# Optimization experiments

Measured on AMD Instinct MI355X. Metric: run time of the kernel, lower is better.

Reference implementation:

```python
import jax, jax.numpy as jnp
import numpy as np

NEG_MASK = -9e15
ALPHA = 0.2  # LeakyReLU negative slope


def _gat_layer(h, adj, W, a):
    # h: [B,K,Fin], adj: [B,K,K], W: [Fin,F], a: [2F]
    Wh = jnp.einsum('bki,io->bko', h, W)            # [B,K,F]
    F = Wh.shape[-1]
    a_src, a_dst = a[:F], a[F:]
    # e_ij = LeakyReLU(a . [Wh_i || Wh_j]) = LeakyReLU(Wh_i.a_src + Wh_j.a_dst)
    f_src = Wh @ a_src                              # [B,K]
    f_dst = Wh @ a_dst                              # [B,K]
    e = jax.nn.leaky_relu(f_src[:, :, None] + f_dst[:, None, :], ALPHA)  # [B,K,K]
    e = jnp.where(adj > 0, e, NEG_MASK)
    att = jax.nn.softmax(e, axis=2)                 # softmax over neighbors j
    # dropout is identity in eval mode (training=False)
    h_prime = jnp.einsum('bkj,bjo->bko', att, Wh)   # [B,K,F]
    return jax.nn.elu(h_prime)


def setup_inputs() -> dict:
    key = jax.random.key(0)
    ks = jax.random.split(key, 6)
    B, K, Fin, H, Fout = 128, 512, 224, 64, 32
    x = jax.random.normal(ks[0], (B, K, Fin), dtype=jnp.float32)
    adj = jax.random.randint(ks[1], (B, K, K), 0, 2, dtype=jnp.int32)
    W1 = jax.random.normal(ks[2], (Fin, H), dtype=jnp.float32) * (1.0 / np.sqrt(Fin))
    a1 = jax.random.normal(ks[3], (2 * H,), dtype=jnp.float32) * 0.1
    W2 = jax.random.normal(ks[4], (H, Fout), dtype=jnp.float32) * (1.0 / np.sqrt(H))
    a2 = jax.random.normal(ks[5], (2 * Fout,), dtype=jnp.float32) * 0.1
    return {"x": x, "adj": adj, "W1": W1, "a1": a1, "W2": W2, "a2": a2}


def reference(x, adj, W1, a1, W2, a2):
    h = _gat_layer(x, adj, W1, a1)   # conv1: in -> hidden
    h = _gat_layer(h, adj, W2, a2)   # conv2: hidden -> out
    return h
```

## Files before the change

kernel.cpp:

```cpp
#include <hip/hip_runtime.h>
#include <stdint.h>


#define B_   128
#define K_   512
#define FIN  224
#define H1   64
#define H2   32

typedef float    f32x4 __attribute__((ext_vector_type(4)));
typedef short    s16x8 __attribute__((ext_vector_type(8)));
typedef unsigned short u16;

__device__ __forceinline__ u16 f2bf(float f){
  uint32_t u = __float_as_uint(f);
  u += 0x7FFFu + ((u >> 16) & 1u);
  return (u16)(u >> 16);
}
__device__ __forceinline__ float bf2f(u16 h){ return __uint_as_float(((uint32_t)h) << 16); }

__device__ __forceinline__ int fragoff(int o, int k, int NO){
  return (((k >> 5) * (NO >> 4) + (o >> 4)) << 9) + (((o & 15) + (((k & 31) >> 3) << 4)) << 3) + (k & 7);
}

__global__ __launch_bounds__(256) void k_bitmask(const int* __restrict__ adj, uint32_t* __restrict__ bits2){
  const int t = threadIdx.x;
#pragma unroll 4
  for (int it = 0; it < 16; ++it){
    const size_t q = (size_t)blockIdx.x * 4096 + it * 256 + t;
    int4 v = reinterpret_cast<const int4*>(adj)[q];
    uint32_t nib = (v.x != 0 ? 1u : 0u) | (v.y != 0 ? 2u : 0u) | (v.z != 0 ? 4u : 0u) | (v.w != 0 ? 8u : 0u);
    uint32_t val = nib << ((t & 7) * 4);
    val |= __shfl_xor(val, 1);
    val |= __shfl_xor(val, 2);
    val |= __shfl_xor(val, 4);
    if ((t & 7) == 0){
      const size_t qw = q >> 3;
      const int st = (int)(qw & 15), i = (int)((qw >> 4) & 511), b = (int)(qw >> 13);
      bits2[((size_t)(b * 16 + st) << 9) + i] = val;
    }
  }
}

__global__ __launch_bounds__(256) void k_prep(const float* __restrict__ W1, const float* __restrict__ W2,
                                              u16* __restrict__ W1F, u16* __restrict__ W2F){
  int t = blockIdx.x * 256 + threadIdx.x;
  if (t < FIN * H1){ int k = t / H1, o = t % H1; W1F[fragoff(o, k, H1)] = f2bf(W1[t]); }
  else { int u = t - FIN * H1; if (u < H1 * H2){ int k = u / H2, o = u % H2; W2F[fragoff(o, k, H2)] = f2bf(W2[u]); } }
}

template<int KD, int NO, bool AF32>
__global__ __launch_bounds__(256) void k_gemm(const void* __restrict__ Ain, const u16* __restrict__ WF,
                                              const float* __restrict__ avec,
                                              u16* __restrict__ WhF, float* __restrict__ fs, float* __restrict__ fd){
  const int tid = threadIdx.x;
  const int wid = tid >> 6, lane = tid & 63;
  const int g = lane >> 4, lr = lane & 15;
  const size_t row0 = (size_t)blockIdx.x * 64;
  const size_t arow = row0 + 16 * wid + lr;

  f32x4 acc[NO / 16];
#pragma unroll
  for (int c = 0; c < NO/16; ++c) acc[c] = (f32x4){0.f, 0.f, 0.f, 0.f};

#pragma unroll
  for (int s = 0; s < KD / 32; ++s){
    const int k0 = s * 32 + 8 * g;
    s16x8 af;
    if (AF32){
      const float* A = (const float*)Ain;
      float4 v0 = *(const float4*)(A + arow * KD + k0);
      float4 v1 = *(const float4*)(A + arow * KD + k0 + 4);
      af[0] = (short)f2bf(v0.x); af[1] = (short)f2bf(v0.y); af[2] = (short)f2bf(v0.z); af[3] = (short)f2bf(v0.w);
      af[4] = (short)f2bf(v1.x); af[5] = (short)f2bf(v1.y); af[6] = (short)f2bf(v1.z); af[7] = (short)f2bf(v1.w);
    } else {
      af = *(const s16x8*)((const u16*)Ain + arow * KD + k0);
    }
#pragma unroll
    for (int c = 0; c < NO/16; ++c){
      const s16x8 bf = *(const s16x8*)(WF + ((s * (NO/16) + c) << 9) + lane * 8);
      acc[c] = __builtin_amdgcn_mfma_f32_16x16x32_bf16(af, bf, acc[c], 0, 0, 0);
    }
  }

  const size_t b = row0 >> 9;
  const int krow0 = (int)(row0 & 511) + 16 * wid + 4 * g;
  float fsp[4] = {0.f,0.f,0.f,0.f}, fdp[4] = {0.f,0.f,0.f,0.f};
#pragma unroll
  for (int c = 0; c < NO/16; ++c){
    const int o = 16 * c + lr;
    const float as = avec[o], ad = avec[NO + o];
#pragma unroll
    for (int r = 0; r < 4; ++r){ fsp[r] += acc[c][r] * as; fdp[r] += acc[c][r] * ad; }
    uint2 pk;
    pk.x = (uint32_t)f2bf(acc[c][0]) | ((uint32_t)f2bf(acc[c][1]) << 16);
    pk.y = (uint32_t)f2bf(acc[c][2]) | ((uint32_t)f2bf(acc[c][3]) << 16);
    *(uint2*)(WhF + b * (NO * 512) + fragoff(o, krow0, NO)) = pk;
  }
#pragma unroll
  for (int m = 1; m < 16; m <<= 1){
#pragma unroll
    for (int r = 0; r < 4; ++r){ fsp[r] += __shfl_xor(fsp[r], m); fdp[r] += __shfl_xor(fdp[r], m); }
  }
  if (lr == 0){
#pragma unroll
    for (int r = 0; r < 4; ++r){
      size_t row = row0 + 16 * wid + 4 * g + r;
      fs[row] = fsp[r]; fd[row] = fdp[r];
    }
  }
}

template<int NO, bool OUTBF>
__global__ __launch_bounds__(256) void k_attn(const u16* __restrict__ WhF, const float* __restrict__ fsv,
                                              const float* __restrict__ fdv, const uint32_t* __restrict__ bits2,
                                              void* __restrict__ outp){
  const int tid = threadIdx.x;
  const int wid = tid >> 6, lane = tid & 63;
  const int g = lane >> 4, lr = lane & 15;
  const int b = blockIdx.x >> 3;
  const int i0 = (blockIdx.x & 7) * 64;
  const int irow = i0 + 16 * wid + lr;
  const float fsr = fsv[(size_t)b * K_ + irow];
  const float* fdb = fdv + (size_t)b * K_;
  const uint32_t* bb = bits2 + ((size_t)b * 16 << 9);
  const u16* whb = WhF + (size_t)b * (NO * 512);

  f32x4 acc[NO / 16];
#pragma unroll
  for (int c = 0; c < NO/16; ++c) acc[c] = (f32x4){0.f, 0.f, 0.f, 0.f};
  float lsum = 0.f;

  for (int st = 0; st < 16; ++st){
    const int j0 = st * 32 + 8 * g;
    const uint32_t byte = (bb[(st << 9) + irow] >> (8 * g)) & 0xFFu;
    float4 fd0 = *(const float4*)(fdb + j0);
    float4 fd1 = *(const float4*)(fdb + j0 + 4);
    float pv[8] = { fd0.x, fd0.y, fd0.z, fd0.w, fd1.x, fd1.y, fd1.z, fd1.w };
    s16x8 bp;
    float lacc = 0.f;
#pragma unroll
    for (int e = 0; e < 8; ++e){
      float sc = fsr + pv[e];
      sc = fmaxf(sc, 0.2f * sc);
      float pe = __expf(sc - 8.0f);
      pe = ((byte >> e) & 1u) ? pe : 0.f;
      u16 h = f2bf(pe);
      bp[e] = (short)h;
      lacc += bf2f(h);
    }
    lsum += lacc;
#pragma unroll
    for (int c = 0; c < NO/16; ++c){
      const s16x8 aw = *(const s16x8*)(whb + ((st * (NO/16) + c) << 9) + lane * 8);
      acc[c] = __builtin_amdgcn_mfma_f32_16x16x32_bf16(aw, bp, acc[c], 0, 0, 0);
    }
  }

  lsum += __shfl_xor(lsum, 16);
  lsum += __shfl_xor(lsum, 32);
  const float inv = 1.0f / lsum;

#pragma unroll
  for (int c = 0; c < NO/16; ++c){
    float v[4];
#pragma unroll
    for (int r = 0; r < 4; ++r){
      float t = acc[c][r] * inv;
      v[r] = t > 0.f ? t : (__expf(t) - 1.0f);
    }
    const size_t base = ((size_t)b * K_ + irow) * NO + 16 * c + 4 * g;
    if (OUTBF){
      uint2 pk;
      pk.x = (uint32_t)f2bf(v[0]) | ((uint32_t)f2bf(v[1]) << 16);
      pk.y = (uint32_t)f2bf(v[2]) | ((uint32_t)f2bf(v[3]) << 16);
      *(uint2*)((u16*)outp + base) = pk;
    } else {
      *(float4*)((float*)outp + base) = (float4){v[0], v[1], v[2], v[3]};
    }
  }
}

extern "C" void kernel_launch(void* const* d_in, const int* in_sizes, int n_in,
                              void* d_out, int out_size, void* d_ws, size_t ws_size,
                              hipStream_t stream){
  const float* x   = (const float*)d_in[0];
  const int*   adj = (const int*)  d_in[1];
  const float* W1  = (const float*)d_in[2];
  const float* a1  = (const float*)d_in[3];
  const float* W2  = (const float*)d_in[4];
  const float* a2  = (const float*)d_in[5];
  float* out = (float*)d_out;

  char* ws = (char*)d_ws;
  u16*      WhF1 = (u16*)     (ws);
  u16*      h1   = (u16*)     (ws + 8388608);
  u16*      WhF2 = (u16*)     (ws + 16777216);
  uint32_t* bits = (uint32_t*)(ws + 20971520);
  float*    fs1  = (float*)   (ws + 25165824);
  float*    fd1  = (float*)   (ws + 25427968);
  float*    fs2  = (float*)   (ws + 25690112);
  float*    fd2  = (float*)   (ws + 25952256);
  u16*      W1F  = (u16*)     (ws + 26214400);
  u16*      W2F  = (u16*)     (ws + 26243072);

  k_bitmask<<<dim3(2048), dim3(256), 0, stream>>>(adj, bits);
  k_prep   <<<dim3(64),   dim3(256), 0, stream>>>(W1, W2, W1F, W2F);
  k_gemm<FIN, H1, true >  <<<dim3(1024), dim3(256), 0, stream>>>((const void*)x,  W1F, a1, WhF1, fs1, fd1);
  k_attn<H1, true >       <<<dim3(1024), dim3(256), 0, stream>>>(WhF1, fs1, fd1, bits, (void*)h1);
  k_gemm<H1,  H2, false>  <<<dim3(1024), dim3(256), 0, stream>>>((const void*)h1, W2F, a2, WhF2, fs2, fd2);
  k_attn<H2, false>       <<<dim3(1024), dim3(256), 0, stream>>>(WhF2, fs2, fd2, bits, (void*)out);
}
```

Measured before the change: 293.9 us.

## Fuse both GAT layers into one per-batch kernel keeping intermediates in LDS

```diff
diff --git a/kernel.cpp b/kernel.cpp
--- a/kernel.cpp
+++ b/kernel.cpp
@@ -2,7 +2,6 @@
 #include <stdint.h>
 
 
-#define B_   128
 #define K_   512
 #define FIN  224
 #define H1   64
@@ -23,160 +22,300 @@
   return (((k >> 5) * (NO >> 4) + (o >> 4)) << 9) + (((o & 15) + (((k & 31) >> 3) << 4)) << 3) + (k & 7);
 }
 
-__global__ __launch_bounds__(256) void k_bitmask(const int* __restrict__ adj, uint32_t* __restrict__ bits2){
-  const int t = threadIdx.x;
+
+__global__ __launch_bounds__(1024, 4) void k_gat(const float* __restrict__ x, const int* __restrict__ adj,
+                                                 const float* __restrict__ W1, const float* __restrict__ a1,
+                                                 const float* __restrict__ W2, const float* __restrict__ a2,
+                                                 float* __restrict__ out){
+  __shared__ __align__(16) char arena[147456];
+  u16*      WhS      = (u16*)     (arena);
+  uint32_t* bits_tmp = (uint32_t*)(arena + 65536);
+  u16*      W1F      = (u16*)     (arena + 98304);
+  u16*      h1S      = (u16*)     (arena + 65536);
+  u16*      W2F      = (u16*)     (arena + 139264);
+  float*    fs_s     = (float*)   (arena + 143360);
+  float*    fd_s     = (float*)   (arena + 145408);
+
+  const int tid = threadIdx.x;
+  const int w = tid >> 6, lane = tid & 63;
+  const int g = lane >> 4, lr = lane & 15;
+  const int b = blockIdx.x;
+
+  for (int e = tid; e < FIN * H1; e += 1024){
+    const int k = e >> 6, o = e & 63;
+    W1F[fragoff(o, k, H1)] = f2bf(W1[e]);
+  }
+#pragma unroll
+  for (int p = 0; p < 2; ++p){
+    const int e = tid + p * 1024;
+    const int k = e >> 5, o = e & 31;
+    W2F[fragoff(o, k, H2)] = f2bf(W2[e]);
+  }
+  {
+    const int4* ap = reinterpret_cast<const int4*>(adj) + (size_t)b * 65536;
 #pragma unroll 4
-  for (int it = 0; it < 16; ++it){
-    const size_t q = (size_t)blockIdx.x * 4096 + it * 256 + t;
-    int4 v = reinterpret_cast<const int4*>(adj)[q];
-    uint32_t nib = (v.x != 0 ? 1u : 0u) | (v.y != 0 ? 2u : 0u) | (v.z != 0 ? 4u : 0u) | (v.w != 0 ? 8u : 0u);
-    uint32_t val = nib << ((t & 7) * 4);
-    val |= __shfl_xor(val, 1);
-    val |= __shfl_xor(val, 2);
-    val |= __shfl_xor(val, 4);
-    if ((t & 7) == 0){
-      const size_t qw = q >> 3;
-      const int st = (int)(qw & 15), i = (int)((qw >> 4) & 511), b = (int)(qw >> 13);
-      bits2[((size_t)(b * 16 + st) << 9) + i] = val;
-    }
-  }
-}
-
-__global__ __launch_bounds__(256) void k_prep(const float* __restrict__ W1, const float* __restrict__ W2,
-                                              u16* __restrict__ W1F, u16* __restrict__ W2F){
-  int t = blockIdx.x * 256 + threadIdx.x;
-  if (t < FIN * H1){ int k = t / H1, o = t % H1; W1F[fragoff(o, k, H1)] = f2bf(W1[t]); }
-  else { int u = t - FIN * H1; if (u < H1 * H2){ int k = u / H2, o = u % H2; W2F[fragoff(o, k, H2)] = f2bf(W2[u]); } }
-}
-
-template<int KD, int NO, bool AF32>
-__global__ __launch_bounds__(256) void k_gemm(const void* __restrict__ Ain, const u16* __restrict__ WF,
-                                              const float* __restrict__ avec,
-                                              u16* __restrict__ WhF, float* __restrict__ fs, float* __restrict__ fd){
-  const int tid = threadIdx.x;
-  const int wid = tid >> 6, lane = tid & 63;
-  const int g = lane >> 4, lr = lane & 15;
-  const size_t row0 = (size_t)blockIdx.x * 64;
-  const size_t arow = row0 + 16 * wid + lr;
-
-  f32x4 acc[NO / 16];
-#pragma unroll
-  for (int c = 0; c < NO/16; ++c) acc[c] = (f32x4){0.f, 0.f, 0.f, 0.f};
-
-#pragma unroll
-  for (int s = 0; s < KD / 32; ++s){
-    const int k0 = s * 32 + 8 * g;
-    s16x8 af;
-    if (AF32){
-      const float* A = (const float*)Ain;
-      float4 v0 = *(const float4*)(A + arow * KD + k0);
-      float4 v1 = *(const float4*)(A + arow * KD + k0 + 4);
-      af[0] = (short)f2bf(v0.x); af[1] = (short)f2bf(v0.y); af[2] = (short)f2bf(v0.z); af[3] = (short)f2bf(v0.w);
-      af[4] = (short)f2bf(v1.x); af[5] = (short)f2bf(v1.y); af[6] = (short)f2bf(v1.z); af[7] = (short)f2bf(v1.w);
-    } else {
-      af = *(const s16x8*)((const u16*)Ain + arow * KD + k0);
-    }
-#pragma unroll
-    for (int c = 0; c < NO/16; ++c){
-      const s16x8 bf = *(const s16x8*)(WF + ((s * (NO/16) + c) << 9) + lane * 8);
-      acc[c] = __builtin_amdgcn_mfma_f32_16x16x32_bf16(af, bf, acc[c], 0, 0, 0);
-    }
-  }
-
-  const size_t b = row0 >> 9;
-  const int krow0 = (int)(row0 & 511) + 16 * wid + 4 * g;
-  float fsp[4] = {0.f,0.f,0.f,0.f}, fdp[4] = {0.f,0.f,0.f,0.f};
-#pragma unroll
-  for (int c = 0; c < NO/16; ++c){
-    const int o = 16 * c + lr;
-    const float as = avec[o], ad = avec[NO + o];
-#pragma unroll
-    for (int r = 0; r < 4; ++r){ fsp[r] += acc[c][r] * as; fdp[r] += acc[c][r] * ad; }
-    uint2 pk;
-    pk.x = (uint32_t)f2bf(acc[c][0]) | ((uint32_t)f2bf(acc[c][1]) << 16);
-    pk.y = (uint32_t)f2bf(acc[c][2]) | ((uint32_t)f2bf(acc[c][3]) << 16);
-    *(uint2*)(WhF + b * (NO * 512) + fragoff(o, krow0, NO)) = pk;
-  }
-#pragma unroll
-  for (int m = 1; m < 16; m <<= 1){
-#pragma unroll
-    for (int r = 0; r < 4; ++r){ fsp[r] += __shfl_xor(fsp[r], m); fdp[r] += __shfl_xor(fdp[r], m); }
-  }
-  if (lr == 0){
-#pragma unroll
-    for (int r = 0; r < 4; ++r){
-      size_t row = row0 + 16 * wid + 4 * g + r;
-      fs[row] = fsp[r]; fd[row] = fdp[r];
-    }
-  }
-}
-
-template<int NO, bool OUTBF>
-__global__ __launch_bounds__(256) void k_attn(const u16* __restrict__ WhF, const float* __restrict__ fsv,
-                                              const float* __restrict__ fdv, const uint32_t* __restrict__ bits2,
-                                              void* __restrict__ outp){
-  const int tid = threadIdx.x;
-  const int wid = tid >> 6, lane = tid & 63;
-  const int g = lane >> 4, lr = lane & 15;
-  const int b = blockIdx.x >> 3;
-  const int i0 = (blockIdx.x & 7) * 64;
-  const int irow = i0 + 16 * wid + lr;
-  const float fsr = fsv[(size_t)b * K_ + irow];
-  const float* fdb = fdv + (size_t)b * K_;
-  const uint32_t* bb = bits2 + ((size_t)b * 16 << 9);
-  const u16* whb = WhF + (size_t)b * (NO * 512);
-
-  f32x4 acc[NO / 16];
-#pragma unroll
-  for (int c = 0; c < NO/16; ++c) acc[c] = (f32x4){0.f, 0.f, 0.f, 0.f};
-  float lsum = 0.f;
-
-  for (int st = 0; st < 16; ++st){
-    const int j0 = st * 32 + 8 * g;
-    const uint32_t byte = (bb[(st << 9) + irow] >> (8 * g)) & 0xFFu;
-    float4 fd0 = *(const float4*)(fdb + j0);
-    float4 fd1 = *(const float4*)(fdb + j0 + 4);
-    float pv[8] = { fd0.x, fd0.y, fd0.z, fd0.w, fd1.x, fd1.y, fd1.z, fd1.w };
-    s16x8 bp;
-    float lacc = 0.f;
-#pragma unroll
-    for (int e = 0; e < 8; ++e){
-      float sc = fsr + pv[e];
-      sc = fmaxf(sc, 0.2f * sc);
-      float pe = __expf(sc - 8.0f);
-      pe = ((byte >> e) & 1u) ? pe : 0.f;
-      u16 h = f2bf(pe);
-      bp[e] = (short)h;
-      lacc += bf2f(h);
-    }
-    lsum += lacc;
-#pragma unroll
-    for (int c = 0; c < NO/16; ++c){
-      const s16x8 aw = *(const s16x8*)(whb + ((st * (NO/16) + c) << 9) + lane * 8);
-      acc[c] = __builtin_amdgcn_mfma_f32_16x16x32_bf16(aw, bp, acc[c], 0, 0, 0);
-    }
-  }
-
-  lsum += __shfl_xor(lsum, 16);
-  lsum += __shfl_xor(lsum, 32);
-  const float inv = 1.0f / lsum;
-
-#pragma unroll
-  for (int c = 0; c < NO/16; ++c){
-    float v[4];
-#pragma unroll
-    for (int r = 0; r < 4; ++r){
-      float t = acc[c][r] * inv;
-      v[r] = t > 0.f ? t : (__expf(t) - 1.0f);
-    }
-    const size_t base = ((size_t)b * K_ + irow) * NO + 16 * c + 4 * g;
-    if (OUTBF){
-      uint2 pk;
-      pk.x = (uint32_t)f2bf(v[0]) | ((uint32_t)f2bf(v[1]) << 16);
-      pk.y = (uint32_t)f2bf(v[2]) | ((uint32_t)f2bf(v[3]) << 16);
-      *(uint2*)((u16*)outp + base) = pk;
-    } else {
-      *(float4*)((float*)outp + base) = (float4){v[0], v[1], v[2], v[3]};
+    for (int it = 0; it < 64; ++it){
+      const int q = it * 1024 + tid;
+      int4 v = ap[q];
+      uint32_t nib = (v.x != 0 ? 1u : 0u) | (v.y != 0 ? 2u : 0u) | (v.z != 0 ? 4u : 0u) | (v.w != 0 ? 8u : 0u);
+      uint32_t val = nib << ((q & 7) * 4);
+      val |= __shfl_xor(val, 1);
+      val |= __shfl_xor(val, 2);
+      val |= __shfl_xor(val, 4);
+      if ((tid & 7) == 0)
+        bits_tmp[((q & 127) >> 3) * K_ + (q >> 7)] = val;
+    }
+  }
+  __syncthreads();
+
+  {
+    f32x4 acc[2][4];
+#pragma unroll
+    for (int h = 0; h < 2; ++h)
+#pragma unroll
+      for (int c = 0; c < 4; ++c) acc[h][c] = (f32x4){0.f,0.f,0.f,0.f};
+
+    for (int s = 0; s < FIN / 32; ++s){
+      s16x8 af[2];
+#pragma unroll
+      for (int h = 0; h < 2; ++h){
+        const float* xr = x + ((size_t)b * K_ + 32 * w + 16 * h + lr) * FIN + s * 32 + 8 * g;
+        float4 v0 = *(const float4*)xr;
+        float4 v1 = *(const float4*)(xr + 4);
+        af[h][0]=(short)f2bf(v0.x); af[h][1]=(short)f2bf(v0.y); af[h][2]=(short)f2bf(v0.z); af[h][3]=(short)f2bf(v0.w);
+        af[h][4]=(short)f2bf(v1.x); af[h][5]=(short)f2bf(v1.y); af[h][6]=(short)f2bf(v1.z); af[h][7]=(short)f2bf(v1.w);
+      }
+#pragma unroll
+      for (int c = 0; c < 4; ++c){
+        const s16x8 bf = *(const s16x8*)&W1F[((s * 4 + c) << 9) + lane * 8];
+#pragma unroll
+        for (int h = 0; h < 2; ++h)
+          acc[h][c] = __builtin_amdgcn_mfma_f32_16x16x32_bf16(af[h], bf, acc[h][c], 0, 0, 0);
+      }
+    }
+    float fsp[2][4] = {{0}}, fdp[2][4] = {{0}};
+#pragma unroll
+    for (int h = 0; h < 2; ++h)
+#pragma unroll
+      for (int c = 0; c < 4; ++c){
+        const int o = 16 * c + lr;
+        const float as = a1[o], ad = a1[H1 + o];
+#pragma unroll
+        for (int r = 0; r < 4; ++r){ fsp[h][r] += acc[h][c][r] * as; fdp[h][r] += acc[h][c][r] * ad; }
+        uint2 pk;
+        pk.x = (uint32_t)f2bf(acc[h][c][0]) | ((uint32_t)f2bf(acc[h][c][1]) << 16);
+        pk.y = (uint32_t)f2bf(acc[h][c][2]) | ((uint32_t)f2bf(acc[h][c][3]) << 16);
+        const int off = ((w * 4 + c) << 9) + ((lr + 16 * (2 * h + (g >> 1))) << 3) + 4 * (g & 1);
+        *(uint2*)&WhS[off] = pk;
+      }
+#pragma unroll
+    for (int m = 1; m < 16; m <<= 1)
+#pragma unroll
+      for (int h = 0; h < 2; ++h)
+#pragma unroll
+        for (int r = 0; r < 4; ++r){ fsp[h][r] += __shfl_xor(fsp[h][r], m); fdp[h][r] += __shfl_xor(fdp[h][r], m); }
+    if (lr == 0){
+#pragma unroll
+      for (int h = 0; h < 2; ++h)
+#pragma unroll
+        for (int r = 0; r < 4; ++r){
+          const int row = 32 * w + 16 * h + 4 * g + r;
+          fs_s[row] = fsp[h][r]; fd_s[row] = fdp[h][r];
+        }
+    }
+  }
+
+  uint32_t bw[2][4] = {{0,0,0,0},{0,0,0,0}};
+#pragma unroll
+  for (int h = 0; h < 2; ++h){
+    const int row = 32 * w + 16 * h + lr;
+#pragma unroll
+    for (int st = 0; st < 16; ++st){
+      const uint32_t byte = (bits_tmp[st * K_ + row] >> (8 * g)) & 0xFFu;
+      bw[h][st >> 2] |= byte << (8 * (st & 3));
+    }
+  }
+  __syncthreads();
+
+  {
+    f32x4 acc[2][4];
+#pragma unroll
+    for (int h = 0; h < 2; ++h)
+#pragma unroll
+      for (int c = 0; c < 4; ++c) acc[h][c] = (f32x4){0.f,0.f,0.f,0.f};
+    float lsum[2] = {0.f, 0.f};
+    const float fsr[2] = { fs_s[32 * w + lr], fs_s[32 * w + 16 + lr] };
+
+    for (int st = 0; st < 16; ++st){
+      const int j0 = 32 * st + 8 * g;
+      float4 fd0 = *(const float4*)&fd_s[j0];
+      float4 fd1 = *(const float4*)&fd_s[j0 + 4];
+      const float pv[8] = { fd0.x, fd0.y, fd0.z, fd0.w, fd1.x, fd1.y, fd1.z, fd1.w };
+      s16x8 bp[2];
+#pragma unroll
+      for (int h = 0; h < 2; ++h){
+        const uint32_t byte = (bw[h][st >> 2] >> (8 * (st & 3))) & 0xFFu;
+        float lacc = 0.f;
+#pragma unroll
+        for (int e = 0; e < 8; ++e){
+          float sc = fsr[h] + pv[e];
+          sc = fmaxf(sc, 0.2f * sc);
+          float pe = __expf(sc - 8.0f);
+          pe = ((byte >> e) & 1u) ? pe : 0.f;
+          u16 hh = f2bf(pe);
+          bp[h][e] = (short)hh;
+          lacc += bf2f(hh);
+        }
+        lsum[h] += lacc;
+      }
+#pragma unroll
+      for (int c = 0; c < 4; ++c){
+        const s16x8 aw = *(const s16x8*)&WhS[((st * 4 + c) << 9) + lane * 8];
+#pragma unroll
+        for (int h = 0; h < 2; ++h)
+          acc[h][c] = __builtin_amdgcn_mfma_f32_16x16x32_bf16(aw, bp[h], acc[h][c], 0, 0, 0);
+      }
+    }
+    float inv[2];
+#pragma unroll
+    for (int h = 0; h < 2; ++h){
+      lsum[h] += __shfl_xor(lsum[h], 16);
+      lsum[h] += __shfl_xor(lsum[h], 32);
+      inv[h] = 1.0f / lsum[h];
+    }
+#pragma unroll
+    for (int h = 0; h < 2; ++h){
+      const int irow = 32 * w + 16 * h + lr;
+#pragma unroll
+      for (int c = 0; c < 4; ++c){
+        float v[4];
+#pragma unroll
+        for (int r = 0; r < 4; ++r){
+          float t = acc[h][c][r] * inv[h];
+          v[r] = t > 0.f ? t : (__expf(t) - 1.0f);
+        }
+        uint2 pk;
+        pk.x = (uint32_t)f2bf(v[0]) | ((uint32_t)f2bf(v[1]) << 16);
+        pk.y = (uint32_t)f2bf(v[2]) | ((uint32_t)f2bf(v[3]) << 16);
+        *(uint2*)&h1S[irow * 72 + 16 * c + 4 * g] = pk;
+      }
+    }
+  }
+  __syncthreads();
+
+  {
+    f32x4 acc[2][2];
+#pragma unroll
+    for (int h = 0; h < 2; ++h)
+#pragma unroll
+      for (int c = 0; c < 2; ++c) acc[h][c] = (f32x4){0.f,0.f,0.f,0.f};
+
+#pragma unroll
+    for (int s = 0; s < H1 / 32; ++s){
+      s16x8 af[2];
+#pragma unroll
+      for (int h = 0; h < 2; ++h)
+        af[h] = *(const s16x8*)&h1S[(32 * w + 16 * h + lr) * 72 + s * 32 + 8 * g];
+#pragma unroll
+      for (int c = 0; c < 2; ++c){
+        const s16x8 bf = *(const s16x8*)&W2F[((s * 2 + c) << 9) + lane * 8];
+#pragma unroll
+        for (int h = 0; h < 2; ++h)
+          acc[h][c] = __builtin_amdgcn_mfma_f32_16x16x32_bf16(af[h], bf, acc[h][c], 0, 0, 0);
+      }
+    }
+    float fsp[2][4] = {{0}}, fdp[2][4] = {{0}};
+#pragma unroll
+    for (int h = 0; h < 2; ++h)
+#pragma unroll
+      for (int c = 0; c < 2; ++c){
+        const int o = 16 * c + lr;
+        const float as = a2[o], ad = a2[H2 + o];
+#pragma unroll
+        for (int r = 0; r < 4; ++r){ fsp[h][r] += acc[h][c][r] * as; fdp[h][r] += acc[h][c][r] * ad; }
+        uint2 pk;
+        pk.x = (uint32_t)f2bf(acc[h][c][0]) | ((uint32_t)f2bf(acc[h][c][1]) << 16);
+        pk.y = (uint32_t)f2bf(acc[h][c][2]) | ((uint32_t)f2bf(acc[h][c][3]) << 16);
+        const int off = ((w * 2 + c) << 9) + ((lr + 16 * (2 * h + (g >> 1))) << 3) + 4 * (g & 1);
+        *(uint2*)&WhS[off] = pk;
+      }
+#pragma unroll
+    for (int m = 1; m < 16; m <<= 1)
+#pragma unroll
+      for (int h = 0; h < 2; ++h)
+#pragma unroll
+        for (int r = 0; r < 4; ++r){ fsp[h][r] += __shfl_xor(fsp[h][r], m); fdp[h][r] += __shfl_xor(fdp[h][r], m); }
+    if (lr == 0){
+#pragma unroll
+      for (int h = 0; h < 2; ++h)
+#pragma unroll
+        for (int r = 0; r < 4; ++r){
+          const int row = 32 * w + 16 * h + 4 * g + r;
+          fs_s[row] = fsp[h][r]; fd_s[row] = fdp[h][r];
+        }
+    }
+  }
+  __syncthreads();
+
+  {
+    f32x4 acc[2][2];
+#pragma unroll
+    for (int h = 0; h < 2; ++h)
+#pragma unroll
+      for (int c = 0; c < 2; ++c) acc[h][c] = (f32x4){0.f,0.f,0.f,0.f};
+    float lsum[2] = {0.f, 0.f};
+    const float fsr[2] = { fs_s[32 * w + lr], fs_s[32 * w + 16 + lr] };
+
+    for (int st = 0; st < 16; ++st){
+      const int j0 = 32 * st + 8 * g;
+      float4 fd0 = *(const float4*)&fd_s[j0];
+      float4 fd1 = *(const float4*)&fd_s[j0 + 4];
+      const float pv[8] = { fd0.x, fd0.y, fd0.z, fd0.w, fd1.x, fd1.y, fd1.z, fd1.w };
+      s16x8 bp[2];
+#pragma unroll
+      for (int h = 0; h < 2; ++h){
+        const uint32_t byte = (bw[h][st >> 2] >> (8 * (st & 3))) & 0xFFu;
+        float lacc = 0.f;
+#pragma unroll
+        for (int e = 0; e < 8; ++e){
+          float sc = fsr[h] + pv[e];
+          sc = fmaxf(sc, 0.2f * sc);
+          float pe = __expf(sc - 8.0f);
+          pe = ((byte >> e) & 1u) ? pe : 0.f;
+          u16 hh = f2bf(pe);
+          bp[h][e] = (short)hh;
+          lacc += bf2f(hh);
+        }
+        lsum[h] += lacc;
+      }
+#pragma unroll
+      for (int c = 0; c < 2; ++c){
+        const s16x8 aw = *(const s16x8*)&WhS[((st * 2 + c) << 9) + lane * 8];
+#pragma unroll
+        for (int h = 0; h < 2; ++h)
+          acc[h][c] = __builtin_amdgcn_mfma_f32_16x16x32_bf16(aw, bp[h], acc[h][c], 0, 0, 0);
+      }
+    }
+    float inv[2];
+#pragma unroll
+    for (int h = 0; h < 2; ++h){
+      lsum[h] += __shfl_xor(lsum[h], 16);
+      lsum[h] += __shfl_xor(lsum[h], 32);
+      inv[h] = 1.0f / lsum[h];
+    }
+#pragma unroll
+    for (int h = 0; h < 2; ++h){
+      const int irow = 32 * w + 16 * h + lr;
+#pragma unroll
+      for (int c = 0; c < 2; ++c){
+        float v[4];
+#pragma unroll
+        for (int r = 0; r < 4; ++r){
+          float t = acc[h][c][r] * inv[h];
+          v[r] = t > 0.f ? t : (__expf(t) - 1.0f);
+        }
+        *(float4*)&out[((size_t)b * K_ + irow) * H2 + 16 * c + 4 * g] = (float4){v[0], v[1], v[2], v[3]};
+      }
     }
   }
 }
@@ -191,23 +330,7 @@
   const float* W2  = (const float*)d_in[4];
   const float* a2  = (const float*)d_in[5];
   float* out = (float*)d_out;
-
-  char* ws = (char*)d_ws;
-  u16*      WhF1 = (u16*)     (ws);
-  u16*      h1   = (u16*)     (ws + 8388608);
-  u16*      WhF2 = (u16*)     (ws + 16777216);
-  uint32_t* bits = (uint32_t*)(ws + 20971520);
-  float*    fs1  = (float*)   (ws + 25165824);
-  float*    fd1  = (float*)   (ws + 25427968);
-  float*    fs2  = (float*)   (ws + 25690112);
-  float*    fd2  = (float*)   (ws + 25952256);
-  u16*      W1F  = (u16*)     (ws + 26214400);
-  u16*      W2F  = (u16*)     (ws + 26243072);
-
-  k_bitmask<<<dim3(2048), dim3(256), 0, stream>>>(adj, bits);
-  k_prep   <<<dim3(64),   dim3(256), 0, stream>>>(W1, W2, W1F, W2F);
-  k_gemm<FIN, H1, true >  <<<dim3(1024), dim3(256), 0, stream>>>((const void*)x,  W1F, a1, WhF1, fs1, fd1);
-  k_attn<H1, true >       <<<dim3(1024), dim3(256), 0, stream>>>(WhF1, fs1, fd1, bits, (void*)h1);
-  k_gemm<H1,  H2, false>  <<<dim3(1024), dim3(256), 0, stream>>>((const void*)h1, W2F, a2, WhF2, fs2, fd2);
-  k_attn<H2, false>       <<<dim3(1024), dim3(256), 0, stream>>>(WhF2, fs2, fd2, bits, (void*)out);
+  (void)d_ws; (void)ws_size;
+
+  k_gat<<<dim3(128), dim3(1024), 0, stream>>>(x, adj, W1, a1, W2, a2, out);
 }
```

New measurement: 323.9 us. +10.2%, slower.
